# Optimization experiments

Measured on AMD Instinct MI355X. Metric: run time of the kernel, lower is better.

## Reference

```python
import jax, jax.numpy as jnp
import numpy as np

N = 50000      # nodes (== input_dim, featureless layer1)
H = 256        # nhidden
L = 8          # nlayers
C = 10         # nclass
E = 1600000    # edges
ALPHA = 0.1
LAMDA = 0.1    # beta in __init__


def setup_inputs() -> dict:
    key = jax.random.key(0)
    ks = jax.random.split(key, 8)
    x = jax.random.normal(ks[0], (N, 1), dtype=jnp.float32)  # unused (featureless)
    rows = jax.random.randint(ks[1], (E,), 0, N, dtype=jnp.int32)
    cols = jax.random.randint(ks[2], (E,), 0, N, dtype=jnp.int32)
    edge_weight = jax.random.uniform(ks[3], (E,), dtype=jnp.float32)
    # parameters
    W1 = jax.random.normal(ks[4], (N, H), dtype=jnp.float32) * 0.05   # layer1.W (randn init)
    stdv = 1.0 / np.sqrt(H)
    Wc = jax.random.uniform(ks[5], (L, H, H), dtype=jnp.float32, minval=-stdv, maxval=stdv)
    W2 = jax.random.normal(ks[6], (H, C), dtype=jnp.float32) * 0.05   # layer2.W
    return {"x": x, "rows": rows, "cols": cols, "edge_weight": edge_weight,
            "W1": W1, "Wc": Wc, "W2": W2}


def reference(x, rows, cols, edge_weight, W1, Wc, W2):
    # eval mode: dropout = identity; x unused (featureless layer1)
    n = W1.shape[0]

    def spmm(X):  # sparse [N,N] @ dense [N,d]
        return jax.ops.segment_sum(edge_weight[:, None] * X[cols], rows, num_segments=n)

    # layer1: adj @ W1, ReLU
    h = jax.nn.relu(spmm(W1))            # [N, H]
    h0 = h
    layer0 = h
    nlayers = Wc.shape[0]
    for i in range(nlayers):
        theta = float(np.log(LAMDA / (i + 1) + 1.0))
        hi = spmm(h)                     # [N, H]
        anchor = h0 if i <= nlayers // 2 else layer0
        support = (1.0 - ALPHA) * hi + ALPHA * anchor
        h = jax.nn.relu(theta * (support @ Wc[i]) + (1.0 - theta) * support)
        if i <= nlayers // 2:
            h0 = h
    # layer2: adj @ (h @ W2)
    return spmm(h @ W2)                  # [N, C]
```

## Files before the change

kernel.cpp:

```cpp
#include <hip/hip_runtime.h>
#include <cmath>

typedef __attribute__((ext_vector_type(8))) short short8v;
typedef __attribute__((ext_vector_type(4))) float float4v;
typedef __attribute__((ext_vector_type(4))) unsigned int u32x4;
typedef unsigned short u16;
typedef unsigned int u32;
typedef unsigned char u8;

#define BCAP 10240

__device__ __forceinline__ u16 f2b(float f) {
  union { float f; u32 u; } v; v.f = f;
  return (u16)((v.u + 0x7fffu + ((v.u >> 16) & 1u)) >> 16);
}
__device__ __forceinline__ float lo_f(u32 u) {
  union { u32 u; float f; } v; v.u = u << 16; return v.f;
}
__device__ __forceinline__ float hi_f(u32 u) {
  union { u32 u; float f; } v; v.u = u & 0xffff0000u; return v.f;
}

__global__ __launch_bounds__(256) void bucketize_kernel(const int* __restrict__ rows,
                                                        const int* __restrict__ cols,
                                                        const float* __restrict__ ew,
                                                        u32* __restrict__ gcur,
                                                        u32* __restrict__ staged_pe,
                                                        u8* __restrict__ staged_row,
                                                        int E, int NB) {
  __shared__ u32 hc[256];
  int tid = threadIdx.x;
  hc[tid] = 0;
  __syncthreads();
  int base = blockIdx.x * 8192;
  for (int k = 0; k < 32; ++k) {
    int i = base + k * 256 + tid;
    if (i < E) atomicAdd(&hc[((u32)rows[i]) >> 8], 1);
  }
  __syncthreads();
  u32 myb = 0;
  u32 mycnt = (tid < NB) ? hc[tid] : 0;
  if (mycnt) myb = atomicAdd(&gcur[tid], mycnt);
  __syncthreads();
  hc[tid] = myb;
  __syncthreads();
  for (int k = 0; k < 32; ++k) {
    int i = base + k * 256 + tid;
    if (i < E) {
      u32 r = (u32)rows[i];
      u32 b = r >> 8;
      u32 pos = atomicAdd(&hc[b], 1);
      if (pos < BCAP) {
        u32 wq = (u32)(ew[i] * 65536.0f);
        if (wq > 65535u) wq = 65535u;
        size_t si = (size_t)b * BCAP + pos;
        staged_pe[si] = (wq << 16) | (u32)cols[i];
        staged_row[si] = (u8)(r & 255u);
      }
    }
  }
}

__global__ __launch_bounds__(256) void bscan_kernel(const u32* __restrict__ gcur,
                                                    u32* __restrict__ bbase, int NB,
                                                    int* __restrict__ rowptrN, int E) {
  __shared__ u32 sd[256];
  int tid = threadIdx.x;
  u32 v = (tid < NB) ? gcur[tid] : 0;
  sd[tid] = v;
  __syncthreads();
  for (int o = 1; o < 256; o <<= 1) {
    u32 t = (tid >= o) ? sd[tid - o] : 0;
    __syncthreads();
    sd[tid] += t;
    __syncthreads();
  }
  if (tid < NB) bbase[tid] = sd[tid] - v;
  if (tid == 0) *rowptrN = E;
}

__global__ __launch_bounds__(256) void bsort_kernel(const u32* __restrict__ gcur,
                                                    const u32* __restrict__ bbase,
                                                    const u32* __restrict__ staged_pe,
                                                    const u8* __restrict__ staged_row,
                                                    u32* __restrict__ pe,
                                                    int* __restrict__ rowptr, int n) {
  __shared__ u32 rh[256];
  __shared__ u32 sd[256];
  __shared__ u32 rcur[256];
  int b = blockIdx.x, tid = threadIdx.x;
  u32 cnt = gcur[b];
  if (cnt > BCAP) cnt = BCAP;
  u32 base = bbase[b];
  rh[tid] = 0;
  __syncthreads();
  const u32* sp = staged_pe + (size_t)b * BCAP;
  const u8* sr = staged_row + (size_t)b * BCAP;
  for (u32 idx = tid; idx < cnt; idx += 256) atomicAdd(&rh[sr[idx]], 1);
  __syncthreads();
  u32 v = rh[tid];
  sd[tid] = v;
  __syncthreads();
  for (int o = 1; o < 256; o <<= 1) {
    u32 t = (tid >= o) ? sd[tid - o] : 0;
    __syncthreads();
    sd[tid] += t;
    __syncthreads();
  }
  u32 excl = sd[tid] - v;
  int gr = b * 256 + tid;
  if (gr < n) rowptr[gr] = (int)(base + excl);
  rcur[tid] = base + excl;
  __syncthreads();
  for (u32 idx = tid; idx < cnt; idx += 256) {
    u32 pos = atomicAdd(&rcur[sr[idx]], 1);
    pe[pos] = sp[idx];
  }
}

__global__ __launch_bounds__(256) void cvt_w1_kernel(const float* __restrict__ in,
                                                     u16* __restrict__ outb, long n4) {
  long i = (long)blockIdx.x * 256 + threadIdx.x;
  if (i >= n4) return;
  float4 v = ((const float4*)in)[i];
  ushort4 r; r.x = f2b(v.x); r.y = f2b(v.y); r.z = f2b(v.z); r.w = f2b(v.w);
  ((ushort4*)outb)[i] = r;
}

__global__ __launch_bounds__(256) void cvt_wc_kernel(const float* __restrict__ in,
                                                     u16* __restrict__ outb) {
  __shared__ u16 t[64][68];
  int l = blockIdx.z;
  int k0 = blockIdx.y << 6, n0 = blockIdx.x << 6;
  float theta = logf(0.1f / (float)(l + 1) + 1.0f);
  float omt = 1.0f - theta;
  int kk = threadIdx.x >> 2;
  int nq = (threadIdx.x & 3) << 4;
  const float* ip = in + ((size_t)l << 16) + ((size_t)(k0 + kk) << 8) + n0 + nq;
  int gk = k0 + kk;
#pragma unroll
  for (int q = 0; q < 16; q += 4) {
    float4 v = *(const float4*)(ip + q);
    float fv[4] = {v.x, v.y, v.z, v.w};
#pragma unroll
    for (int x = 0; x < 4; ++x) {
      int gn = n0 + nq + q + x;
      float f = theta * fv[x];
      if (gk == gn) f += omt;
      t[nq + q + x][kk] = f2b(f);
    }
  }
  __syncthreads();
  int nn = threadIdx.x >> 2;
  int kq = (threadIdx.x & 3) << 4;
  u16* op = outb + ((size_t)l << 16) + ((size_t)(n0 + nn) << 8) + k0 + kq;
  u32x4 w0, w1;
#pragma unroll
  for (int x = 0; x < 4; ++x) {
    w0[x] = (u32)t[nn][kq + 2 * x] | ((u32)t[nn][kq + 2 * x + 1] << 16);
    w1[x] = (u32)t[nn][kq + 8 + 2 * x] | ((u32)t[nn][kq + 8 + 2 * x + 1] << 16);
  }
  *(u32x4*)op = w0;
  *(u32x4*)(op + 8) = w1;
}

__global__ __launch_bounds__(256, 6) void spmm1_kernel(const int* __restrict__ rowptr,
                                                       const u32* __restrict__ pe,
                                                       const u16* __restrict__ X,
                                                       u16* __restrict__ outb, int n) {
  int row = blockIdx.x * 4 + (threadIdx.x >> 6);
  if (row >= n) return;
  int lane = threadIdx.x & 63;
  int half = lane >> 5;
  int cq = lane & 31;
  int s = rowptr[row], e = rowptr[row + 1];
  float a[8] = {0, 0, 0, 0, 0, 0, 0, 0};
  for (int j2 = s; j2 < e; j2 += 16) {
    u32 p[8];
#pragma unroll
    for (int u = 0; u < 8; ++u) {
      int j = j2 + 2 * u + half;
      p[u] = __builtin_nontemporal_load(pe + ((j < e) ? j : (e - 1)));
    }
    u32x4 v[8];
#pragma unroll
    for (int u = 0; u < 8; ++u)
      v[u] = *(const u32x4*)(X + ((size_t)(p[u] & 0xFFFFu) << 8) + (cq << 3));
#pragma unroll
    for (int u = 0; u < 8; ++u) {
      float wv = (float)(p[u] >> 16) * (1.0f / 65536.0f);
      if (j2 + 2 * u + half >= e) wv = 0.f;
#pragma unroll
      for (int q = 0; q < 4; ++q) {
        a[2 * q] = fmaf(wv, lo_f(v[u][q]), a[2 * q]);
        a[2 * q + 1] = fmaf(wv, hi_f(v[u][q]), a[2 * q + 1]);
      }
    }
  }
#pragma unroll
  for (int q = 0; q < 8; ++q) a[q] += __shfl_xor(a[q], 32);
  if (lane < 32) {
    u32x4 o;
#pragma unroll
    for (int q = 0; q < 4; ++q)
      o[q] = (u32)f2b(fmaxf(a[2 * q], 0.f)) | ((u32)f2b(fmaxf(a[2 * q + 1], 0.f)) << 16);
    __builtin_nontemporal_store(o, (u32x4*)(outb + ((size_t)row << 8) + (cq << 3)));
  }
}

__global__ __launch_bounds__(256, 6) void spmm_blend_kernel(const int* __restrict__ rowptr,
                                                            const u32* __restrict__ pe,
                                                            const u16* __restrict__ X,
                                                            const u16* __restrict__ anchor,
                                                            u16* __restrict__ outb, int n) {
  int row = blockIdx.x * 4 + (threadIdx.x >> 6);
  if (row >= n) return;
  int lane = threadIdx.x & 63;
  int half = lane >> 5;
  int cq = lane & 31;
  int s = rowptr[row], e = rowptr[row + 1];
  float a[8] = {0, 0, 0, 0, 0, 0, 0, 0};
  for (int j2 = s; j2 < e; j2 += 16) {
    u32 p[8];
#pragma unroll
    for (int u = 0; u < 8; ++u) {
      int j = j2 + 2 * u + half;
      p[u] = __builtin_nontemporal_load(pe + ((j < e) ? j : (e - 1)));
    }
    u32x4 v[8];
#pragma unroll
    for (int u = 0; u < 8; ++u)
      v[u] = *(const u32x4*)(X + ((size_t)(p[u] & 0xFFFFu) << 8) + (cq << 3));
#pragma unroll
    for (int u = 0; u < 8; ++u) {
      float wv = (float)(p[u] >> 16) * (1.0f / 65536.0f);
      if (j2 + 2 * u + half >= e) wv = 0.f;
#pragma unroll
      for (int q = 0; q < 4; ++q) {
        a[2 * q] = fmaf(wv, lo_f(v[u][q]), a[2 * q]);
        a[2 * q + 1] = fmaf(wv, hi_f(v[u][q]), a[2 * q + 1]);
      }
    }
  }
#pragma unroll
  for (int q = 0; q < 8; ++q) a[q] += __shfl_xor(a[q], 32);
  if (lane < 32) {
    size_t off = ((size_t)row << 8) + (cq << 3);
    u32x4 av = __builtin_nontemporal_load((const u32x4*)(anchor + off));
    u32x4 o;
#pragma unroll
    for (int q = 0; q < 4; ++q) {
      float r0 = 0.9f * a[2 * q] + 0.1f * lo_f(av[q]);
      float r1 = 0.9f * a[2 * q + 1] + 0.1f * hi_f(av[q]);
      o[q] = (u32)f2b(r0) | ((u32)f2b(r1) << 16);
    }
    __builtin_nontemporal_store(o, (u32x4*)(outb + off));
  }
}

__global__ __launch_bounds__(128) void gemm_kernel(const u16* __restrict__ A,
                                                   const u16* __restrict__ B,
                                                   u16* __restrict__ Hout) {
  __shared__ u16 tile[64 * 264];
  int wave = threadIdx.x >> 6;
  int lane = threadIdx.x & 63;
  int m0 = blockIdx.x * 64 + wave * 32;
  int r0 = m0 + (lane & 15);
  int khalf = (lane >> 4) << 3;
  const u16* Ap = A + ((size_t)r0 << 8) + khalf;
  const u16* Bp = B + ((lane & 15) << 8) + khalf;

  float4v acc0[16], acc1[16];
#pragma unroll
  for (int i = 0; i < 16; ++i) {
    acc0[i] = (float4v){0.f, 0.f, 0.f, 0.f};
    acc1[i] = (float4v){0.f, 0.f, 0.f, 0.f};
  }
#pragma unroll
  for (int ks = 0; ks < 8; ++ks) {
    short8v a0 = *(const short8v*)(Ap + (ks << 5));
    short8v a1 = *(const short8v*)(Ap + 4096 + (ks << 5));
#pragma unroll
    for (int nf = 0; nf < 16; ++nf) {
      short8v b = *(const short8v*)(Bp + (nf << 12) + (ks << 5));
      acc0[nf] = __builtin_amdgcn_mfma_f32_16x16x32_bf16(a0, b, acc0[nf], 0, 0, 0);
      acc1[nf] = __builtin_amdgcn_mfma_f32_16x16x32_bf16(a1, b, acc1[nf], 0, 0, 0);
    }
  }
  int lrbase = wave * 32 + ((lane >> 4) << 2);
  int ccol = lane & 15;
#pragma unroll
  for (int nf = 0; nf < 16; ++nf) {
    int col = (nf << 4) + ccol;
#pragma unroll
    for (int j = 0; j < 4; ++j) {
      tile[(lrbase + j) * 264 + col] = f2b(fmaxf(acc0[nf][j], 0.f));
      tile[(lrbase + j + 16) * 264 + col] = f2b(fmaxf(acc1[nf][j], 0.f));
    }
  }
  __syncthreads();
#pragma unroll
  for (int it = 0; it < 16; ++it) {
    int idx = it * 128 + threadIdx.x;
    int lr = idx >> 5;
    int ch = idx & 31;
    u32x4 v = *(const u32x4*)(tile + lr * 264 + (ch << 3));
    __builtin_nontemporal_store(
        v, (u32x4*)(Hout + (((size_t)blockIdx.x * 64 + lr) << 8) + (ch << 3)));
  }
}

__global__ __launch_bounds__(256) void gemm2_kernel(const u16* __restrict__ Hb,
                                                    const float* __restrict__ W2,
                                                    float* __restrict__ g, int n) {
  __shared__ float sW2[2560];
  for (int i = threadIdx.x; i < 2560; i += 256) sW2[i] = W2[i];
  __syncthreads();
  int idx = blockIdx.x * 256 + threadIdx.x;
  if (idx >= n * 10) return;
  int r = idx / 10, c = idx - r * 10;
  const u16* hp = Hb + ((size_t)r << 8);
  float acc = 0.f;
  for (int k = 0; k < 256; k += 8) {
    u32x4 v = *(const u32x4*)(hp + k);
#pragma unroll
    for (int q = 0; q < 4; ++q) {
      acc = fmaf(lo_f(v[q]), sW2[(k + 2 * q) * 10 + c], acc);
      acc = fmaf(hi_f(v[q]), sW2[(k + 2 * q + 1) * 10 + c], acc);
    }
  }
  g[idx] = acc;
}

__global__ __launch_bounds__(256) void spmm_final_kernel(const int* __restrict__ rowptr,
                                                         const u32* __restrict__ pe,
                                                         const float* __restrict__ g,
                                                         float* __restrict__ out, int n) {
  int row = blockIdx.x * 4 + (threadIdx.x >> 6);
  if (row >= n) return;
  int lane = threadIdx.x & 63;
  int es = lane / 10;
  int c = lane - es * 10;
  bool active = lane < 60;
  int s = rowptr[row], e = rowptr[row + 1];
  float acc = 0.f;
  for (int j6 = s; j6 < e; j6 += 24) {
#pragma unroll
    for (int u = 0; u < 4; ++u) {
      int j = j6 + 6 * u + es;
      int jc = (j < e) ? j : (e - 1);
      u32 p = __builtin_nontemporal_load(pe + jc);
      float wv = (float)(p >> 16) * (1.0f / 65536.0f);
      if (!active || j >= e) wv = 0.f;
      acc = fmaf(wv, g[(size_t)(p & 0xFFFFu) * 10 + c], acc);
    }
  }
  float a0 = acc;
  acc = a0 + __shfl(a0, lane + 10, 64) + __shfl(a0, lane + 20, 64) +
        __shfl(a0, lane + 30, 64) + __shfl(a0, lane + 40, 64) + __shfl(a0, lane + 50, 64);
  if (lane < 10) out[(size_t)row * 10 + lane] = acc;
}

extern "C" void kernel_launch(void* const* d_in, const int* in_sizes, int n_in,
                              void* d_out, int out_size, void* d_ws, size_t ws_size,
                              hipStream_t stream) {
  const int* rows = (const int*)d_in[1];
  const int* cols = (const int*)d_in[2];
  const float* ew = (const float*)d_in[3];
  const float* W1 = (const float*)d_in[4];
  const float* Wc = (const float*)d_in[5];
  const float* W2 = (const float*)d_in[6];
  float* out = (float*)d_out;
  const int N = in_sizes[0];
  const int E = in_sizes[1];
  const int L = in_sizes[5] >> 16;
  const int NP = ((N + 127) / 128) * 128;
  const int NB = (N + 255) >> 8;

  char* w = (char*)d_ws;
  size_t off = 0;
  auto carve = [&](size_t bytes) -> char* {
    char* p = w + off;
    off = (off + bytes + 255) & ~(size_t)255;
    return p;
  };
  int* rowptr = (int*)carve(((size_t)N + 1) * 4);
  u32* gcur = (u32*)carve(256 * 4);
  u32* bbase = (u32*)carve(256 * 4);
  u32* pe = (u32*)carve((size_t)E * 4);
  u16* Wcb = (u16*)carve((size_t)L * 65536 * 2);
  u16* layer0 = (u16*)carve((size_t)NP * 512);
  u16* bufA = (u16*)carve((size_t)NP * 512);
  u16* bufB = (u16*)carve((size_t)NP * 512);
  u16* suppt = (u16*)carve((size_t)NP * 512);
  float* g = (float*)carve((size_t)NP * 40);
  u16* W1b = (u16*)carve((size_t)NP * 512);
  u32* staged_pe = (u32*)suppt;
  u8* staged_row = (u8*)suppt + (size_t)NB * BCAP * 4;

  int nb4 = (N + 3) / 4;

  (void)hipMemsetAsync(gcur, 0, 256 * 4, stream);
  bucketize_kernel<<<(E + 8191) / 8192, 256, 0, stream>>>(rows, cols, ew, gcur,
                                                          staged_pe, staged_row, E, NB);
  bscan_kernel<<<1, 256, 0, stream>>>(gcur, bbase, NB, rowptr + N, E);
  bsort_kernel<<<NB, 256, 0, stream>>>(gcur, bbase, staged_pe, staged_row, pe, rowptr, N);

  cvt_wc_kernel<<<dim3(4, 4, L), 256, 0, stream>>>(Wc, Wcb);
  {
    long n4 = (long)N * 64;
    cvt_w1_kernel<<<(int)((n4 + 255) / 256), 256, 0, stream>>>(W1, W1b, n4);
  }

  spmm1_kernel<<<nb4, 256, 0, stream>>>(rowptr, pe, W1b, layer0, N);

  const u16* hin = layer0;
  int half = L / 2;
  for (int i = 0; i < L; ++i) {
    const u16* anchor = (i <= half) ? hin : layer0;
    spmm_blend_kernel<<<nb4, 256, 0, stream>>>(rowptr, pe, hin, anchor, suppt, N);
    u16* hout = (hin == bufA) ? bufB : ((hin == bufB) ? bufA : bufB);
    gemm_kernel<<<NP / 64, 128, 0, stream>>>(suppt, Wcb + (size_t)i * 65536, hout);
    hin = hout;
  }

  gemm2_kernel<<<(N * 10 + 255) / 256, 256, 0, stream>>>(hin, W2, g, N);
  spmm_final_kernel<<<nb4, 256, 0, stream>>>(rowptr, pe, g, out, N);
}
```

Measured before the change: 1.499 ms.

## Store node features in 32-column panels to localize SpMM gathers

Feature matrices are stored as 8 column panels of 32 bf16 values per node instead of full 256-wide rows, and SpMM kernels now process one panel per block with 8 edges in flight per wave. The aim is to shrink the randomly gathered working set per panel so it stays in L2 rather than spilling to the larger last-level cache. The GEMM, conversion, and final projection kernels are adapted to read/write the panel layout. The trade-off is reading the edge list and row pointers 8 times per layer and more shuffle reductions.

Result: slower. 2.122 ms (+41.6%).

```diff
diff --git a/kernel.cpp b/kernel.cpp
--- a/kernel.cpp
+++ b/kernel.cpp
@@ -4,6 +4,7 @@
 typedef __attribute__((ext_vector_type(8))) short short8v;
 typedef __attribute__((ext_vector_type(4))) float float4v;
 typedef __attribute__((ext_vector_type(4))) unsigned int u32x4;
+typedef __attribute__((ext_vector_type(2))) unsigned int u32x2;
 typedef unsigned short u16;
 typedef unsigned int u32;
 typedef unsigned char u8;
@@ -119,12 +120,15 @@
 }
 
 __global__ __launch_bounds__(256) void cvt_w1_kernel(const float* __restrict__ in,
-                                                     u16* __restrict__ outb, long n4) {
-  long i = (long)blockIdx.x * 256 + threadIdx.x;
-  if (i >= n4) return;
-  float4 v = ((const float4*)in)[i];
-  ushort4 r; r.x = f2b(v.x); r.y = f2b(v.y); r.z = f2b(v.z); r.w = f2b(v.w);
-  ((ushort4*)outb)[i] = r;
+                                                     u16* __restrict__ outb, int n, int NP) {
+  int tid = blockIdx.x * 256 + threadIdx.x;
+  if (tid >= n * 8) return;
+  int node = tid >> 3, q = tid & 7, panel = blockIdx.y;
+  float4 v = *(const float4*)(in + (size_t)node * 256 + panel * 32 + q * 4);
+  u32x2 o;
+  o[0] = (u32)f2b(v.x) | ((u32)f2b(v.y) << 16);
+  o[1] = (u32)f2b(v.z) | ((u32)f2b(v.w) << 16);
+  *(u32x2*)(outb + ((size_t)panel * NP + node) * 32 + q * 4) = o;
 }
 
 __global__ __launch_bounds__(256) void cvt_wc_kernel(const float* __restrict__ in,
@@ -164,110 +168,116 @@
   *(u32x4*)(op + 8) = w1;
 }
 
-__global__ __launch_bounds__(256, 6) void spmm1_kernel(const int* __restrict__ rowptr,
-                                                       const u32* __restrict__ pe,
-                                                       const u16* __restrict__ X,
-                                                       u16* __restrict__ outb, int n) {
-  int row = blockIdx.x * 4 + (threadIdx.x >> 6);
+__global__ __launch_bounds__(256) void spmm1_kernel(const int* __restrict__ rowptr,
+                                                    const u32* __restrict__ pe,
+                                                    const u16* __restrict__ Xp,
+                                                    u16* __restrict__ outp, int n, int NP) {
+  int bid = blockIdx.x;
+  int panel = bid & 7;
+  int row = (bid >> 3) * 4 + (threadIdx.x >> 6);
   if (row >= n) return;
   int lane = threadIdx.x & 63;
-  int half = lane >> 5;
-  int cq = lane & 31;
+  int slot = lane >> 3, cl = lane & 7;
+  const u16* X = Xp + (size_t)panel * NP * 32;
   int s = rowptr[row], e = rowptr[row + 1];
-  float a[8] = {0, 0, 0, 0, 0, 0, 0, 0};
-  for (int j2 = s; j2 < e; j2 += 16) {
-    u32 p[8];
-#pragma unroll
-    for (int u = 0; u < 8; ++u) {
-      int j = j2 + 2 * u + half;
-      p[u] = __builtin_nontemporal_load(pe + ((j < e) ? j : (e - 1)));
-    }
-    u32x4 v[8];
-#pragma unroll
-    for (int u = 0; u < 8; ++u)
-      v[u] = *(const u32x4*)(X + ((size_t)(p[u] & 0xFFFFu) << 8) + (cq << 3));
-#pragma unroll
-    for (int u = 0; u < 8; ++u) {
-      float wv = (float)(p[u] >> 16) * (1.0f / 65536.0f);
-      if (j2 + 2 * u + half >= e) wv = 0.f;
-#pragma unroll
-      for (int q = 0; q < 4; ++q) {
-        a[2 * q] = fmaf(wv, lo_f(v[u][q]), a[2 * q]);
-        a[2 * q + 1] = fmaf(wv, hi_f(v[u][q]), a[2 * q + 1]);
-      }
-    }
-  }
-#pragma unroll
-  for (int q = 0; q < 8; ++q) a[q] += __shfl_xor(a[q], 32);
-  if (lane < 32) {
-    u32x4 o;
-#pragma unroll
-    for (int q = 0; q < 4; ++q)
-      o[q] = (u32)f2b(fmaxf(a[2 * q], 0.f)) | ((u32)f2b(fmaxf(a[2 * q + 1], 0.f)) << 16);
-    __builtin_nontemporal_store(o, (u32x4*)(outb + ((size_t)row << 8) + (cq << 3)));
-  }
-}
-
-__global__ __launch_bounds__(256, 6) void spmm_blend_kernel(const int* __restrict__ rowptr,
-                                                            const u32* __restrict__ pe,
-                                                            const u16* __restrict__ X,
-                                                            const u16* __restrict__ anchor,
-                                                            u16* __restrict__ outb, int n) {
-  int row = blockIdx.x * 4 + (threadIdx.x >> 6);
+  float a0 = 0, a1 = 0, a2 = 0, a3 = 0;
+  for (int j0 = s; j0 < e; j0 += 32) {
+    u32 p[4];
+#pragma unroll
+    for (int g = 0; g < 4; ++g) {
+      int j = j0 + (g << 3) + slot;
+      p[g] = __builtin_nontemporal_load(pe + ((j < e) ? j : (e - 1)));
+    }
+    u32x2 v[4];
+#pragma unroll
+    for (int g = 0; g < 4; ++g)
+      v[g] = *(const u32x2*)(X + ((size_t)(p[g] & 0xFFFFu) << 5) + (cl << 2));
+#pragma unroll
+    for (int g = 0; g < 4; ++g) {
+      float wv = (float)(p[g] >> 16) * (1.0f / 65536.0f);
+      if (j0 + (g << 3) + slot >= e) wv = 0.f;
+      a0 = fmaf(wv, lo_f(v[g][0]), a0);
+      a1 = fmaf(wv, hi_f(v[g][0]), a1);
+      a2 = fmaf(wv, lo_f(v[g][1]), a2);
+      a3 = fmaf(wv, hi_f(v[g][1]), a3);
+    }
+  }
+#pragma unroll
+  for (int m = 8; m < 64; m <<= 1) {
+    a0 += __shfl_xor(a0, m); a1 += __shfl_xor(a1, m);
+    a2 += __shfl_xor(a2, m); a3 += __shfl_xor(a3, m);
+  }
+  if (lane < 8) {
+    u32x2 o;
+    o[0] = (u32)f2b(fmaxf(a0, 0.f)) | ((u32)f2b(fmaxf(a1, 0.f)) << 16);
+    o[1] = (u32)f2b(fmaxf(a2, 0.f)) | ((u32)f2b(fmaxf(a3, 0.f)) << 16);
+    __builtin_nontemporal_store(
+        o, (u32x2*)(outp + ((size_t)panel * NP + row) * 32 + (cl << 2)));
+  }
+}
+
+__global__ __launch_bounds__(256) void spmm_blend_kernel(const int* __restrict__ rowptr,
+                                                         const u32* __restrict__ pe,
+                                                         const u16* __restrict__ Xp,
+                                                         const u16* __restrict__ anchor,
+                                                         u16* __restrict__ outp,
+                                                         int n, int NP) {
+  int bid = blockIdx.x;
+  int panel = bid & 7;
+  int row = (bid >> 3) * 4 + (threadIdx.x >> 6);
   if (row >= n) return;
   int lane = threadIdx.x & 63;
-  int half = lane >> 5;
-  int cq = lane & 31;
+  int slot = lane >> 3, cl = lane & 7;
+  const u16* X = Xp + (size_t)panel * NP * 32;
   int s = rowptr[row], e = rowptr[row + 1];
-  float a[8] = {0, 0, 0, 0, 0, 0, 0, 0};
-  for (int j2 = s; j2 < e; j2 += 16) {
-    u32 p[8];
-#pragma unroll
-    for (int u = 0; u < 8; ++u) {
-      int j = j2 + 2 * u + half;
-      p[u] = __builtin_nontemporal_load(pe + ((j < e) ? j : (e - 1)));
-    }
-    u32x4 v[8];
-#pragma unroll
-    for (int u = 0; u < 8; ++u)
-      v[u] = *(const u32x4*)(X + ((size_t)(p[u] & 0xFFFFu) << 8) + (cq << 3));
-#pragma unroll
-    for (int u = 0; u < 8; ++u) {
-      float wv = (float)(p[u] >> 16) * (1.0f / 65536.0f);
-      if (j2 + 2 * u + half >= e) wv = 0.f;
-#pragma unroll
-      for (int q = 0; q < 4; ++q) {
-        a[2 * q] = fmaf(wv, lo_f(v[u][q]), a[2 * q]);
-        a[2 * q + 1] = fmaf(wv, hi_f(v[u][q]), a[2 * q + 1]);
-      }
-    }
-  }
-#pragma unroll
-  for (int q = 0; q < 8; ++q) a[q] += __shfl_xor(a[q], 32);
-  if (lane < 32) {
-    size_t off = ((size_t)row << 8) + (cq << 3);
-    u32x4 av = __builtin_nontemporal_load((const u32x4*)(anchor + off));
-    u32x4 o;
-#pragma unroll
-    for (int q = 0; q < 4; ++q) {
-      float r0 = 0.9f * a[2 * q] + 0.1f * lo_f(av[q]);
-      float r1 = 0.9f * a[2 * q + 1] + 0.1f * hi_f(av[q]);
-      o[q] = (u32)f2b(r0) | ((u32)f2b(r1) << 16);
-    }
-    __builtin_nontemporal_store(o, (u32x4*)(outb + off));
+  float a0 = 0, a1 = 0, a2 = 0, a3 = 0;
+  for (int j0 = s; j0 < e; j0 += 32) {
+    u32 p[4];
+#pragma unroll
+    for (int g = 0; g < 4; ++g) {
+      int j = j0 + (g << 3) + slot;
+      p[g] = __builtin_nontemporal_load(pe + ((j < e) ? j : (e - 1)));
+    }
+    u32x2 v[4];
+#pragma unroll
+    for (int g = 0; g < 4; ++g)
+      v[g] = *(const u32x2*)(X + ((size_t)(p[g] & 0xFFFFu) << 5) + (cl << 2));
+#pragma unroll
+    for (int g = 0; g < 4; ++g) {
+      float wv = (float)(p[g] >> 16) * (1.0f / 65536.0f);
+      if (j0 + (g << 3) + slot >= e) wv = 0.f;
+      a0 = fmaf(wv, lo_f(v[g][0]), a0);
+      a1 = fmaf(wv, hi_f(v[g][0]), a1);
+      a2 = fmaf(wv, lo_f(v[g][1]), a2);
+      a3 = fmaf(wv, hi_f(v[g][1]), a3);
+    }
+  }
+#pragma unroll
+  for (int m = 8; m < 64; m <<= 1) {
+    a0 += __shfl_xor(a0, m); a1 += __shfl_xor(a1, m);
+    a2 += __shfl_xor(a2, m); a3 += __shfl_xor(a3, m);
+  }
+  if (lane < 8) {
+    size_t off = ((size_t)panel * NP + row) * 32 + (cl << 2);
+    u32x2 av = __builtin_nontemporal_load((const u32x2*)(anchor + off));
+    u32x2 o;
+    o[0] = (u32)f2b(0.9f * a0 + 0.1f * lo_f(av[0])) |
+           ((u32)f2b(0.9f * a1 + 0.1f * hi_f(av[0])) << 16);
+    o[1] = (u32)f2b(0.9f * a2 + 0.1f * lo_f(av[1])) |
+           ((u32)f2b(0.9f * a3 + 0.1f * hi_f(av[1])) << 16);
+    __builtin_nontemporal_store(o, (u32x2*)(outp + off));
   }
 }
 
 __global__ __launch_bounds__(128) void gemm_kernel(const u16* __restrict__ A,
                                                    const u16* __restrict__ B,
-                                                   u16* __restrict__ Hout) {
+                                                   u16* __restrict__ Hout, int NP) {
   __shared__ u16 tile[64 * 264];
   int wave = threadIdx.x >> 6;
   int lane = threadIdx.x & 63;
   int m0 = blockIdx.x * 64 + wave * 32;
   int r0 = m0 + (lane & 15);
   int khalf = (lane >> 4) << 3;
-  const u16* Ap = A + ((size_t)r0 << 8) + khalf;
   const u16* Bp = B + ((lane & 15) << 8) + khalf;
 
   float4v acc0[16], acc1[16];
@@ -278,8 +288,9 @@
   }
 #pragma unroll
   for (int ks = 0; ks < 8; ++ks) {
-    short8v a0 = *(const short8v*)(Ap + (ks << 5));
-    short8v a1 = *(const short8v*)(Ap + 4096 + (ks << 5));
+    const u16* Ap = A + ((size_t)ks * NP + r0) * 32 + khalf;
+    short8v a0 = *(const short8v*)Ap;
+    short8v a1 = *(const short8v*)(Ap + 512);
 #pragma unroll
     for (int nf = 0; nf < 16; ++nf) {
       short8v b = *(const short8v*)(Bp + (nf << 12) + (ks << 5));
@@ -302,31 +313,44 @@
 #pragma unroll
   for (int it = 0; it < 16; ++it) {
     int idx = it * 128 + threadIdx.x;
-    int lr = idx >> 5;
-    int ch = idx & 31;
-    u32x4 v = *(const u32x4*)(tile + lr * 264 + (ch << 3));
+    int quad = idx & 3;
+    int lr = (idx >> 2) & 63;
+    int panel = idx >> 8;
+    u32x4 v = *(const u32x4*)(tile + lr * 264 + (panel << 5) + (quad << 3));
     __builtin_nontemporal_store(
-        v, (u32x4*)(Hout + (((size_t)blockIdx.x * 64 + lr) << 8) + (ch << 3)));
+        v, (u32x4*)(Hout + ((size_t)panel * NP + (size_t)blockIdx.x * 64 + lr) * 32 +
+                    (quad << 3)));
   }
 }
 
 __global__ __launch_bounds__(256) void gemm2_kernel(const u16* __restrict__ Hb,
                                                     const float* __restrict__ W2,
-                                                    float* __restrict__ g, int n) {
+                                                    float* __restrict__ g, int n, int NP) {
   __shared__ float sW2[2560];
   for (int i = threadIdx.x; i < 2560; i += 256) sW2[i] = W2[i];
   __syncthreads();
   int idx = blockIdx.x * 256 + threadIdx.x;
   if (idx >= n * 10) return;
   int r = idx / 10, c = idx - r * 10;
-  const u16* hp = Hb + ((size_t)r << 8);
   float acc = 0.f;
-  for (int k = 0; k < 256; k += 8) {
-    u32x4 v = *(const u32x4*)(hp + k);
+#pragma unroll
+  for (int p = 0; p < 8; ++p) {
+    const u16* bp = Hb + ((size_t)p * NP + r) * 32;
+    const float* wp = sW2 + p * 320 + c;
+    u32x4 v0 = *(const u32x4*)bp;
+    u32x4 v1 = *(const u32x4*)(bp + 8);
+    u32x4 v2 = *(const u32x4*)(bp + 16);
+    u32x4 v3 = *(const u32x4*)(bp + 24);
 #pragma unroll
     for (int q = 0; q < 4; ++q) {
-      acc = fmaf(lo_f(v[q]), sW2[(k + 2 * q) * 10 + c], acc);
-      acc = fmaf(hi_f(v[q]), sW2[(k + 2 * q + 1) * 10 + c], acc);
+      acc = fmaf(lo_f(v0[q]), wp[(2 * q) * 10], acc);
+      acc = fmaf(hi_f(v0[q]), wp[(2 * q + 1) * 10], acc);
+      acc = fmaf(lo_f(v1[q]), wp[(8 + 2 * q) * 10], acc);
+      acc = fmaf(hi_f(v1[q]), wp[(8 + 2 * q + 1) * 10], acc);
+      acc = fmaf(lo_f(v2[q]), wp[(16 + 2 * q) * 10], acc);
+      acc = fmaf(hi_f(v2[q]), wp[(16 + 2 * q + 1) * 10], acc);
+      acc = fmaf(lo_f(v3[q]), wp[(24 + 2 * q) * 10], acc);
+      acc = fmaf(hi_f(v3[q]), wp[(24 + 2 * q + 1) * 10], acc);
     }
   }
   g[idx] = acc;
@@ -395,8 +419,8 @@
   u16* suppt = (u16*)carve((size_t)NP * 512);
   float* g = (float*)carve((size_t)NP * 40);
   u16* W1b = (u16*)carve((size_t)NP * 512);
-  u32* staged_pe = (u32*)suppt;
-  u8* staged_row = (u8*)suppt + (size_t)NB * BCAP * 4;
+  u32* staged_pe = (u32*)((void*)bufA);
+  u8* staged_row = (u8*)bufA + (size_t)NB * BCAP * 4;
 
   int nb4 = (N + 3) / 4;
 
@@ -407,23 +431,20 @@
   bsort_kernel<<<NB, 256, 0, stream>>>(gcur, bbase, staged_pe, staged_row, pe, rowptr, N);
 
   cvt_wc_kernel<<<dim3(4, 4, L), 256, 0, stream>>>(Wc, Wcb);
-  {
-    long n4 = (long)N * 64;
-    cvt_w1_kernel<<<(int)((n4 + 255) / 256), 256, 0, stream>>>(W1, W1b, n4);
-  }
-
-  spmm1_kernel<<<nb4, 256, 0, stream>>>(rowptr, pe, W1b, layer0, N);
+  cvt_w1_kernel<<<dim3((N * 8 + 255) / 256, 8), 256, 0, stream>>>(W1, W1b, N, NP);
+
+  spmm1_kernel<<<nb4 * 8, 256, 0, stream>>>(rowptr, pe, W1b, layer0, N, NP);
 
   const u16* hin = layer0;
   int half = L / 2;
   for (int i = 0; i < L; ++i) {
     const u16* anchor = (i <= half) ? hin : layer0;
-    spmm_blend_kernel<<<nb4, 256, 0, stream>>>(rowptr, pe, hin, anchor, suppt, N);
+    spmm_blend_kernel<<<nb4 * 8, 256, 0, stream>>>(rowptr, pe, hin, anchor, suppt, N, NP);
     u16* hout = (hin == bufA) ? bufB : ((hin == bufB) ? bufA : bufB);
-    gemm_kernel<<<NP / 64, 128, 0, stream>>>(suppt, Wcb + (size_t)i * 65536, hout);
+    gemm_kernel<<<NP / 64, 128, 0, stream>>>(suppt, Wcb + (size_t)i * 65536, hout, NP);
     hin = hout;
   }
 
-  gemm2_kernel<<<(N * 10 + 255) / 256, 256, 0, stream>>>(hin, W2, g, N);
+  gemm2_kernel<<<(N * 10 + 255) / 256, 256, 0, stream>>>(hin, W2, g, N, NP);
   spmm_final_kernel<<<nb4, 256, 0, stream>>>(rowptr, pe, g, out, N);
 }
```
